# Kernel optimization log

Hardware: AMD Instinct MI355X
Metric: run time of the kernel (lower is better)

The kernel has to match this reference:

```python
import jax, jax.numpy as jnp
import numpy as np

THRESH = 0.3

def _quantize_ternary(s):
    # straight-through ternary: forward value is q, gradient is identity
    q = jnp.where(s > THRESH, 1.0, jnp.where(s < -THRESH, -1.0, 0.0))
    return s + jax.lax.stop_gradient(q - s)

def setup_inputs() -> dict:
    key = jax.random.key(0)
    k1, k2, k3 = jax.random.split(key, 3)
    B, D, T, C = 32768, 1024, 16, 1000
    x = jax.random.normal(k1, (B, D), dtype=jnp.float32)
    sigs_raw = jax.random.normal(k2, (T, D), dtype=jnp.float32) * 0.5
    # per-tile Linear(d_model, n_classes): weight [C, D], bias [C]
    W = jax.random.normal(k3, (T, C, D), dtype=jnp.float32) / np.sqrt(D)
    b = jnp.zeros((T, C), dtype=jnp.float32)
    return {"x": x, "sigs_raw": sigs_raw, "W": W, "b": b}

def reference(x, sigs_raw, W, b):
    sigs = _quantize_ternary(sigs_raw)          # [T, D] ternary values
    scores = x @ sigs.T                          # [B, T]
    tile_indices = jnp.argmax(scores, axis=-1)   # [B] top-1 routing
    n_tiles = W.shape[0]
    logits = jnp.zeros((x.shape[0], W.shape[1]), dtype=x.dtype)  # [B, C]
    # static loop over tiles: masked per-expert linear, combined by select
    for t in range(n_tiles):
        m = (tile_indices == t)[:, None]         # [B, 1]
        yt = x @ W[t].T + b[t]                   # [B, C]
        logits = jnp.where(m, yt, logits)
    return logits, tile_indices
```

## Files before the change

### kernel.cpp

```cpp
#include <hip/hip_runtime.h>

#define NBROWS 32768
#define ND 1024
#define NT 16
#define NC 1000
#define NHB 128
#define MAX_RB128 272

typedef short short8 __attribute__((ext_vector_type(8)));
typedef float f32x4 __attribute__((ext_vector_type(4)));
typedef unsigned short ushort_t;

typedef __attribute__((address_space(1))) const unsigned int* gas_t;
typedef __attribute__((address_space(3))) unsigned int* las_t;

__device__ __forceinline__ void async_copy16(const void* g, void* l) {
  __builtin_amdgcn_global_load_lds((gas_t)g, (las_t)l, 16, 0, 0);
}

__device__ __forceinline__ unsigned f2bf(float f) {
  unsigned u = __float_as_uint(f);
  u += 0x7FFFu + ((u >> 16) & 1u);
  return u >> 16;
}
__device__ __forceinline__ unsigned pk2(float a, float b) {
  return f2bf(a) | (f2bf(b) << 16);
}
__device__ __forceinline__ int swz(int row) { return (row & 3) ^ ((row >> 2) & 3); }

__global__ __launch_bounds__(512) void fused_pre(
    const float* __restrict__ x, const float* __restrict__ sigs_raw,
    int* __restrict__ tidx, float* __restrict__ out_idx,
    const float* __restrict__ W, ushort_t* __restrict__ wbf) {
  __shared__ signed char s_lds[NT * ND];
  int tid = threadIdx.x;
  int bid = blockIdx.x;
  if (bid >= 4096) {
    if (!wbf) return;
    size_t e = (((size_t)(bid - 4096)) * 512 + tid) * 8;
    int t = (int)(e >> 20);
    int rem = (int)(e & 1048575);
    int col = rem >> 10, k = rem & 1023;
    uint4 o;
    if (col < NC) {
      const float* src = W + ((size_t)t * NC + col) * ND + k;
      float4 a = *(const float4*)src;
      float4 b = *(const float4*)(src + 4);
      o = make_uint4(pk2(a.x, a.y), pk2(a.z, a.w), pk2(b.x, b.y), pk2(b.z, b.w));
    } else {
      o = make_uint4(0, 0, 0, 0);
    }
    *(uint4*)(wbf + e) = o;
    return;
  }
  for (int i = tid; i < NT * ND; i += 512) {
    float s = sigs_raw[i];
    s_lds[i] = (s > 0.3f) ? 1 : ((s < -0.3f) ? -1 : 0);
  }
  __syncthreads();
  int lane = tid & 63;
  int row = bid * 8 + (tid >> 6);
  const float* xr = x + (size_t)row * ND + lane * 16;
  float4 v0 = *(const float4*)(xr);
  float4 v1 = *(const float4*)(xr + 4);
  float4 v2 = *(const float4*)(xr + 8);
  float4 v3 = *(const float4*)(xr + 12);
  float xv[16] = {v0.x, v0.y, v0.z, v0.w, v1.x, v1.y, v1.z, v1.w,
                  v2.x, v2.y, v2.z, v2.w, v3.x, v3.y, v3.z, v3.w};
  float best = 0.0f;
  int bt = 0;
#pragma unroll
  for (int t = 0; t < NT; t++) {
    int4 sc = *(const int4*)(s_lds + t * ND + lane * 16);
    int wa[4] = {sc.x, sc.y, sc.z, sc.w};
    float p = 0.0f;
#pragma unroll
    for (int wi = 0; wi < 4; wi++)
#pragma unroll
      for (int bi = 0; bi < 4; bi++)
        p = fmaf((float)(signed char)(wa[wi] >> (8 * bi)), xv[wi * 4 + bi], p);
#pragma unroll
    for (int o = 32; o > 0; o >>= 1) p += __shfl_xor(p, o);
    if (t == 0 || p > best) { best = p; bt = t; }
  }
  if (lane == 0) {
    tidx[row] = bt;
    out_idx[row] = (float)bt;
  }
}

__global__ __launch_bounds__(256) void trix_hist(const int* __restrict__ tidx,
                                                 int* __restrict__ blkhist) {
  __shared__ int h[NT];
  int tid = threadIdx.x;
  if (tid < NT) h[tid] = 0;
  __syncthreads();
  int t = tidx[blockIdx.x * 256 + tid];
  atomicAdd(&h[t], 1);
  __syncthreads();
  if (tid < NT) blkhist[blockIdx.x * NT + tid] = h[tid];
}

__global__ __launch_bounds__(256) void trix_prefix(const int* __restrict__ blkhist,
                                                   int* __restrict__ blkbase,
                                                   int* __restrict__ meta) {
  __shared__ int part[NT][16];
  int tid = threadIdx.x;
  int t = tid >> 4, g = tid & 15;
  int s = 0;
  for (int b = g; b < NHB; b += 16) s += blkhist[b * NT + t];
  part[t][g] = s;
  __syncthreads();
  if (tid == 0) {
    int off = 0, cb2 = 0;
    for (int tt = 0; tt < NT; tt++) {
      int c = 0;
#pragma unroll
      for (int gg = 0; gg < 16; gg++) c += part[tt][gg];
      meta[tt] = c;
      meta[16 + tt] = off;
      meta[50 + tt] = cb2;
      off += c;
      cb2 += (c + 127) >> 7;
    }
    meta[32] = off;
    meta[66] = cb2;
  }
  __syncthreads();
  if (tid < NT) {
    int run = meta[16 + tid];
    for (int b = 0; b < NHB; b++) {
      blkbase[b * NT + tid] = run;
      run += blkhist[b * NT + tid];
    }
  }
}

__global__ __launch_bounds__(256) void trix_scatter(const int* __restrict__ tidx,
                                                    const int* __restrict__ blkbase,
                                                    int* __restrict__ rowlist) {
  __shared__ int h[NT];
  int tid = threadIdx.x;
  if (tid < NT) h[tid] = 0;
  __syncthreads();
  int row = blockIdx.x * 256 + tid;
  int t = tidx[row];
  int r = atomicAdd(&h[t], 1);
  rowlist[blkbase[blockIdx.x * NT + t] + r] = row;
}

__global__ __launch_bounds__(512) void trix_gather(const float* __restrict__ x,
                                                   const int* __restrict__ rowlist,
                                                   ushort_t* __restrict__ xsrt) {
  int tid = threadIdx.x;
  int lane = tid & 63, wv = tid >> 6;
  int p = blockIdx.x * 8 + wv;
  int row = rowlist[p];
  const float* src = x + (size_t)row * ND + lane * 16;
  float4 v0 = *(const float4*)(src);
  float4 v1 = *(const float4*)(src + 4);
  float4 v2 = *(const float4*)(src + 8);
  float4 v3 = *(const float4*)(src + 12);
  ushort_t* dst = xsrt + (size_t)p * ND + lane * 16;
  *(uint4*)(dst) = make_uint4(pk2(v0.x, v0.y), pk2(v0.z, v0.w), pk2(v1.x, v1.y), pk2(v1.z, v1.w));
  *(uint4*)(dst + 8) = make_uint4(pk2(v2.x, v2.y), pk2(v2.z, v2.w), pk2(v3.x, v3.y), pk2(v3.z, v3.w));
}

__global__ __launch_bounds__(256, 3) void trix_gemm4(
    const ushort_t* __restrict__ xsrt, const ushort_t* __restrict__ wbf,
    const float* __restrict__ bias, const int* __restrict__ meta,
    const int* __restrict__ rowlist, float* __restrict__ out) {
  __shared__ __align__(16) ushort_t A_lds[128 * 64];
  __shared__ __align__(16) ushort_t B_lds[128 * 64];
  __shared__ int rl[128];
  int bid = blockIdx.x;
  int w = (bid & 7) * 272 + (bid >> 3);
  int nb = w & 7, rb = w >> 3;
  if (rb >= meta[66]) return;
  int t = 0;
  while (t < NT - 1 && rb >= meta[51 + t]) t++;
  int row0 = meta[16 + t] + (rb - meta[50 + t]) * 128;
  int cnt = meta[17 + t] - row0;
  if (cnt > 128) cnt = 128;
  int tid = threadIdx.x;
  if (tid < 128) rl[tid] = rowlist[(tid < cnt) ? (row0 + tid) : row0];

  int lane = tid & 63, wv = tid >> 6;
  int srow = lane >> 3;
  int schunk = ((lane & 7) ^ srow) * 8;
  const ushort_t* aSrc = xsrt + (size_t)(row0 + wv * 32 + srow) * ND + schunk;
  const ushort_t* bSrc =
      wbf + ((size_t)t << 20) + (size_t)(nb * 128 + wv * 32 + srow) * ND + schunk;
  ushort_t* aDst = A_lds + wv * 32 * 64 + lane * 8;
  ushort_t* bDst = B_lds + wv * 32 * 64 + lane * 8;

  int wr = wv >> 1, wc = wv & 1;
  int rsel = lane & 15, ksl = lane >> 4, rx = rsel & 7;
  int sl0 = (ksl ^ rx) * 8;
  int sl1 = ((4 + ksl) ^ rx) * 8;
  int aoff = (wr * 64 + rsel) * 64;
  int boff = (wc * 64 + rsel) * 64;

  f32x4 acc[4][4] = {};

#pragma unroll 1
  for (int k0 = 0; k0 < ND; k0 += 64) {
#pragma unroll
    for (int j = 0; j < 4; j++) {
      async_copy16(aSrc + k0 + j * 8 * ND, aDst + j * 512);
      async_copy16(bSrc + k0 + j * 8 * ND, bDst + j * 512);
    }
    __syncthreads();
    short8 af[4][2], bf2[2][2];
#pragma unroll
    for (int m = 0; m < 4; m++) {
      af[m][0] = *(const short8*)(A_lds + aoff + m * 1024 + sl0);
      af[m][1] = *(const short8*)(A_lds + aoff + m * 1024 + sl1);
    }
#pragma unroll
    for (int nh = 0; nh < 2; nh++) {
#pragma unroll
      for (int j = 0; j < 2; j++) {
        int n = nh * 2 + j;
        bf2[j][0] = *(const short8*)(B_lds + boff + n * 1024 + sl0);
        bf2[j][1] = *(const short8*)(B_lds + boff + n * 1024 + sl1);
      }
#pragma unroll
      for (int m = 0; m < 4; m++)
#pragma unroll
        for (int j = 0; j < 2; j++) {
          acc[m][nh * 2 + j] = __builtin_amdgcn_mfma_f32_16x16x32_bf16(
              af[m][0], bf2[j][0], acc[m][nh * 2 + j], 0, 0, 0);
          acc[m][nh * 2 + j] = __builtin_amdgcn_mfma_f32_16x16x32_bf16(
              af[m][1], bf2[j][1], acc[m][nh * 2 + j], 0, 0, 0);
        }
    }
    __syncthreads();
  }

  float bv[4];
  int bcol[4];
#pragma unroll
  for (int n = 0; n < 4; ++n) {
    bcol[n] = nb * 128 + wc * 64 + n * 16 + rsel;
    bv[n] = (bcol[n] < NC) ? bias[t * NC + bcol[n]] : 0.0f;
  }
#pragma unroll
  for (int m = 0; m < 4; ++m) {
#pragma unroll
    for (int r = 0; r < 4; ++r) {
      int lr = wr * 64 + m * 16 + ksl * 4 + r;
      if (lr < cnt) {
        size_t ob = (size_t)rl[lr] * NC;
#pragma unroll
        for (int n = 0; n < 4; ++n)
          if (bcol[n] < NC) out[ob + bcol[n]] = acc[m][n][r] + bv[n];
      }
    }
  }
}

__global__ __launch_bounds__(256) void trix_gemm_fb(
    const float* __restrict__ x, const float* __restrict__ W,
    const float* __restrict__ bias, const int* __restrict__ meta,
    const int* __restrict__ rowlist, float* __restrict__ out) {
  __shared__ __align__(16) unsigned char aT[128 * 64];
  __shared__ __align__(16) unsigned char bT[128 * 64];
  __shared__ int rl[128];
  int nb = blockIdx.x, rb = blockIdx.y;
  if (rb >= meta[66]) return;
  int t = 0;
  while (t < NT - 1 && rb >= meta[51 + t]) t++;
  int row0 = meta[16 + t] + (rb - meta[50 + t]) * 128;
  int cnt = meta[17 + t] - row0;
  if (cnt > 128) cnt = 128;
  int tid = threadIdx.x;
  if (tid < 128) rl[tid] = rowlist[(tid < cnt) ? (row0 + tid) : row0];
  __syncthreads();
  int half = tid & 1, rloc = tid >> 1;
  const float* xp = x + (size_t)rl[rloc] * ND + half * 16;
  int wn = nb * 128 + rloc;
  if (wn > NC - 1) wn = NC - 1;
  const float* wp = W + ((size_t)t * NC + wn) * ND + half * 16;
  int sw = swz(rloc);
  unsigned char* aw0 = aT + rloc * 64 + (((half * 2 + 0) ^ sw) << 4);
  unsigned char* aw1 = aT + rloc * 64 + (((half * 2 + 1) ^ sw) << 4);
  unsigned char* bw0 = bT + rloc * 64 + (((half * 2 + 0) ^ sw) << 4);
  unsigned char* bw1 = bT + rloc * 64 + (((half * 2 + 1) ^ sw) << 4);
  int lane = tid & 63, wv = tid >> 6;
  int wr = wv >> 1, wc = wv & 1;
  int rsel = lane & 15, slot = lane >> 4;
  f32x4 acc[4][4] = {};
  for (int k0 = 0; k0 < ND; k0 += 32) {
    const float* xk = xp + k0;
    const float* wk = wp + k0;
    float4 a0 = *(const float4*)(xk);
    float4 a1 = *(const float4*)(xk + 4);
    float4 a2 = *(const float4*)(xk + 8);
    float4 a3 = *(const float4*)(xk + 12);
    float4 b0 = *(const float4*)(wk);
    float4 b1 = *(const float4*)(wk + 4);
    float4 b2 = *(const float4*)(wk + 8);
    float4 b3 = *(const float4*)(wk + 12);
    *(uint4*)aw0 = make_uint4(pk2(a0.x, a0.y), pk2(a0.z, a0.w), pk2(a1.x, a1.y), pk2(a1.z, a1.w));
    *(uint4*)aw1 = make_uint4(pk2(a2.x, a2.y), pk2(a2.z, a2.w), pk2(a3.x, a3.y), pk2(a3.z, a3.w));
    *(uint4*)bw0 = make_uint4(pk2(b0.x, b0.y), pk2(b0.z, b0.w), pk2(b1.x, b1.y), pk2(b1.z, b1.w));
    *(uint4*)bw1 = make_uint4(pk2(b2.x, b2.y), pk2(b2.z, b2.w), pk2(b3.x, b3.y), pk2(b3.z, b3.w));
    __syncthreads();
    short8 af2[4], bfr[4];
#pragma unroll
    for (int i = 0; i < 4; i++) {
      int arr = wr * 64 + i * 16 + rsel;
      af2[i] = *(const short8*)(aT + arr * 64 + ((slot ^ swz(arr)) << 4));
      int brr = wc * 64 + i * 16 + rsel;
      bfr[i] = *(const short8*)(bT + brr * 64 + ((slot ^ swz(brr)) << 4));
    }
#pragma unroll
    for (int mi = 0; mi < 4; mi++)
#pragma unroll
      for (int ni = 0; ni < 4; ni++)
        acc[mi][ni] = __builtin_amdgcn_mfma_f32_16x16x32_bf16(af2[mi], bfr[ni], acc[mi][ni], 0, 0, 0);
    __syncthreads();
  }
#pragma unroll
  for (int mi = 0; mi < 4; mi++) {
#pragma unroll
    for (int r = 0; r < 4; r++) {
      int rloc2 = wr * 64 + mi * 16 + slot * 4 + r;
      if (rloc2 < cnt) {
        size_t obase = (size_t)rl[rloc2] * NC;
#pragma unroll
        for (int ni = 0; ni < 4; ni++) {
          int col = nb * 128 + wc * 64 + ni * 16 + rsel;
          if (col < NC) out[obase + col] = acc[mi][ni][r] + bias[t * NC + col];
        }
      }
    }
  }
}

extern "C" void kernel_launch(void* const* d_in, const int* in_sizes, int n_in,
                              void* d_out, int out_size, void* d_ws, size_t ws_size,
                              hipStream_t stream) {
  const float* x = (const float*)d_in[0];
  const float* sigs = (const float*)d_in[1];
  const float* W = (const float*)d_in[2];
  const float* bias = (const float*)d_in[3];
  float* out = (float*)d_out;

  const size_t XSRT_B = (size_t)(NBROWS + 256) * ND * 2;
  const size_t WBF_B = (size_t)NT * 1024 * ND * 2;
  bool fast = ws_size >= XSRT_B + WBF_B + (1 << 20);

  char* wsb = (char*)d_ws;
  ushort_t* xsrt = nullptr;
  ushort_t* wbf = nullptr;
  int* tidx;
  if (fast) {
    xsrt = (ushort_t*)wsb;
    wbf = (ushort_t*)(wsb + XSRT_B);
    tidx = (int*)(wsb + XSRT_B + WBF_B);
  } else {
    tidx = (int*)wsb;
  }
  int* rowlist = tidx + NBROWS;
  int* meta = rowlist + NBROWS;
  int* blkhist = meta + 80;
  int* blkbase = blkhist + NHB * NT;

  fused_pre<<<8192, 512, 0, stream>>>(x, sigs, tidx, out + (size_t)NBROWS * NC, W, wbf);
  trix_hist<<<NHB, 256, 0, stream>>>(tidx, blkhist);
  trix_prefix<<<1, 256, 0, stream>>>(blkhist, blkbase, meta);
  trix_scatter<<<NHB, 256, 0, stream>>>(tidx, blkbase, rowlist);
  if (fast) {
    trix_gather<<<NBROWS / 8, 512, 0, stream>>>(x, rowlist, xsrt);
    trix_gemm4<<<8 * MAX_RB128, 256, 0, stream>>>(xsrt, wbf, bias, meta, rowlist, out);
  } else {
    trix_gemm_fb<<<dim3(8, MAX_RB128), 256, 0, stream>>>(x, W, bias, meta, rowlist, out);
  }
}
```

Measured before the change: 218.8 us.

## Fuse bf16 x conversion into routing pass and double-buffer GEMM LDS tiles

```diff
diff --git a/kernel.cpp b/kernel.cpp
--- a/kernel.cpp
+++ b/kernel.cpp
@@ -31,7 +31,8 @@
 __global__ __launch_bounds__(512) void fused_pre(
     const float* __restrict__ x, const float* __restrict__ sigs_raw,
     int* __restrict__ tidx, float* __restrict__ out_idx,
-    const float* __restrict__ W, ushort_t* __restrict__ wbf) {
+    const float* __restrict__ W, ushort_t* __restrict__ wbf,
+    ushort_t* __restrict__ xbf) {
   __shared__ signed char s_lds[NT * ND];
   int tid = threadIdx.x;
   int bid = blockIdx.x;
@@ -67,6 +68,11 @@
   float4 v3 = *(const float4*)(xr + 12);
   float xv[16] = {v0.x, v0.y, v0.z, v0.w, v1.x, v1.y, v1.z, v1.w,
                   v2.x, v2.y, v2.z, v2.w, v3.x, v3.y, v3.z, v3.w};
+  if (xbf) {
+    ushort_t* xo = xbf + (size_t)row * ND + lane * 16;
+    *(uint4*)(xo) = make_uint4(pk2(v0.x, v0.y), pk2(v0.z, v0.w), pk2(v1.x, v1.y), pk2(v1.z, v1.w));
+    *(uint4*)(xo + 8) = make_uint4(pk2(v2.x, v2.y), pk2(v2.z, v2.w), pk2(v3.x, v3.y), pk2(v3.z, v3.w));
+  }
   float best = 0.0f;
   int bt = 0;
 #pragma unroll
@@ -149,29 +155,12 @@
   rowlist[blkbase[blockIdx.x * NT + t] + r] = row;
 }
 
-__global__ __launch_bounds__(512) void trix_gather(const float* __restrict__ x,
-                                                   const int* __restrict__ rowlist,
-                                                   ushort_t* __restrict__ xsrt) {
-  int tid = threadIdx.x;
-  int lane = tid & 63, wv = tid >> 6;
-  int p = blockIdx.x * 8 + wv;
-  int row = rowlist[p];
-  const float* src = x + (size_t)row * ND + lane * 16;
-  float4 v0 = *(const float4*)(src);
-  float4 v1 = *(const float4*)(src + 4);
-  float4 v2 = *(const float4*)(src + 8);
-  float4 v3 = *(const float4*)(src + 12);
-  ushort_t* dst = xsrt + (size_t)p * ND + lane * 16;
-  *(uint4*)(dst) = make_uint4(pk2(v0.x, v0.y), pk2(v0.z, v0.w), pk2(v1.x, v1.y), pk2(v1.z, v1.w));
-  *(uint4*)(dst + 8) = make_uint4(pk2(v2.x, v2.y), pk2(v2.z, v2.w), pk2(v3.x, v3.y), pk2(v3.z, v3.w));
-}
-
-__global__ __launch_bounds__(256, 3) void trix_gemm4(
-    const ushort_t* __restrict__ xsrt, const ushort_t* __restrict__ wbf,
+__global__ __launch_bounds__(256, 2) void trix_gemm5(
+    const ushort_t* __restrict__ xbf, const ushort_t* __restrict__ wbf,
     const float* __restrict__ bias, const int* __restrict__ meta,
     const int* __restrict__ rowlist, float* __restrict__ out) {
-  __shared__ __align__(16) ushort_t A_lds[128 * 64];
-  __shared__ __align__(16) ushort_t B_lds[128 * 64];
+  __shared__ __align__(16) ushort_t A_lds[2][128 * 64];
+  __shared__ __align__(16) ushort_t B_lds[2][128 * 64];
   __shared__ int rl[128];
   int bid = blockIdx.x;
   int w = (bid & 7) * 272 + (bid >> 3);
@@ -184,15 +173,19 @@
   if (cnt > 128) cnt = 128;
   int tid = threadIdx.x;
   if (tid < 128) rl[tid] = rowlist[(tid < cnt) ? (row0 + tid) : row0];
+  __syncthreads();
 
   int lane = tid & 63, wv = tid >> 6;
   int srow = lane >> 3;
   int schunk = ((lane & 7) ^ srow) * 8;
-  const ushort_t* aSrc = xsrt + (size_t)(row0 + wv * 32 + srow) * ND + schunk;
-  const ushort_t* bSrc =
-      wbf + ((size_t)t << 20) + (size_t)(nb * 128 + wv * 32 + srow) * ND + schunk;
-  ushort_t* aDst = A_lds + wv * 32 * 64 + lane * 8;
-  ushort_t* bDst = B_lds + wv * 32 * 64 + lane * 8;
+  const ushort_t* aS[4];
+  const ushort_t* bS[4];
+#pragma unroll
+  for (int j = 0; j < 4; j++) {
+    aS[j] = xbf + (size_t)rl[wv * 32 + j * 8 + srow] * ND + schunk;
+    bS[j] = wbf + ((size_t)t << 20) + (size_t)(nb * 128 + wv * 32 + j * 8 + srow) * ND + schunk;
+  }
+  int ldst = wv * 2048 + lane * 8;
 
   int wr = wv >> 1, wc = wv & 1;
   int rsel = lane & 15, ksl = lane >> 4, rx = rsel & 7;
@@ -203,38 +196,45 @@
 
   f32x4 acc[4][4] = {};
 
+#define STAGE(DB, KTL)                                       \
+  _Pragma("unroll") for (int j = 0; j < 4; j++) {            \
+    async_copy16(aS[j] + (KTL) * 64, &A_lds[DB][ldst + j * 512]); \
+    async_copy16(bS[j] + (KTL) * 64, &B_lds[DB][ldst + j * 512]); \
+  }
+
+#define COMPUTE(DB)                                                          \
+  {                                                                          \
+    short8 af[4][2], bf2[2][2];                                              \
+    _Pragma("unroll") for (int m = 0; m < 4; m++) {                          \
+      af[m][0] = *(const short8*)(&A_lds[DB][aoff + m * 1024 + sl0]);        \
+      af[m][1] = *(const short8*)(&A_lds[DB][aoff + m * 1024 + sl1]);        \
+    }                                                                        \
+    _Pragma("unroll") for (int nh = 0; nh < 2; nh++) {                       \
+      _Pragma("unroll") for (int j = 0; j < 2; j++) {                        \
+        int n = nh * 2 + j;                                                  \
+        bf2[j][0] = *(const short8*)(&B_lds[DB][boff + n * 1024 + sl0]);     \
+        bf2[j][1] = *(const short8*)(&B_lds[DB][boff + n * 1024 + sl1]);     \
+      }                                                                      \
+      _Pragma("unroll") for (int m = 0; m < 4; m++)                          \
+          _Pragma("unroll") for (int j = 0; j < 2; j++) {                    \
+        acc[m][nh * 2 + j] = __builtin_amdgcn_mfma_f32_16x16x32_bf16(        \
+            af[m][0], bf2[j][0], acc[m][nh * 2 + j], 0, 0, 0);               \
+        acc[m][nh * 2 + j] = __builtin_amdgcn_mfma_f32_16x16x32_bf16(        \
+            af[m][1], bf2[j][1], acc[m][nh * 2 + j], 0, 0, 0);               \
+      }                                                                      \
+    }                                                                        \
+  }
+
+  STAGE(0, 0);
+  __syncthreads();
+
 #pragma unroll 1
-  for (int k0 = 0; k0 < ND; k0 += 64) {
-#pragma unroll
-    for (int j = 0; j < 4; j++) {
-      async_copy16(aSrc + k0 + j * 8 * ND, aDst + j * 512);
-      async_copy16(bSrc + k0 + j * 8 * ND, bDst + j * 512);
-    }
+  for (int kt = 0; kt < 8; ++kt) {
+    STAGE(1, 2 * kt + 1);
+    COMPUTE(0);
     __syncthreads();
-    short8 af[4][2], bf2[2][2];
-#pragma unroll
-    for (int m = 0; m < 4; m++) {
-      af[m][0] = *(const short8*)(A_lds + aoff + m * 1024 + sl0);
-      af[m][1] = *(const short8*)(A_lds + aoff + m * 1024 + sl1);
-    }
-#pragma unroll
-    for (int nh = 0; nh < 2; nh++) {
-#pragma unroll
-      for (int j = 0; j < 2; j++) {
-        int n = nh * 2 + j;
-        bf2[j][0] = *(const short8*)(B_lds + boff + n * 1024 + sl0);
-        bf2[j][1] = *(const short8*)(B_lds + boff + n * 1024 + sl1);
-      }
-#pragma unroll
-      for (int m = 0; m < 4; m++)
-#pragma unroll
-        for (int j = 0; j < 2; j++) {
-          acc[m][nh * 2 + j] = __builtin_amdgcn_mfma_f32_16x16x32_bf16(
-              af[m][0], bf2[j][0], acc[m][nh * 2 + j], 0, 0, 0);
-          acc[m][nh * 2 + j] = __builtin_amdgcn_mfma_f32_16x16x32_bf16(
-              af[m][1], bf2[j][1], acc[m][nh * 2 + j], 0, 0, 0);
-        }
-    }
+    if (kt < 7) STAGE(0, 2 * kt + 2);
+    COMPUTE(1);
     __syncthreads();
   }
 
@@ -258,6 +258,8 @@
       }
     }
   }
+#undef STAGE
+#undef COMPUTE
 }
 
 __global__ __launch_bounds__(256) void trix_gemm_fb(
@@ -348,18 +350,18 @@
   const float* bias = (const float*)d_in[3];
   float* out = (float*)d_out;
 
-  const size_t XSRT_B = (size_t)(NBROWS + 256) * ND * 2;
+  const size_t XBF_B = (size_t)NBROWS * ND * 2;
   const size_t WBF_B = (size_t)NT * 1024 * ND * 2;
-  bool fast = ws_size >= XSRT_B + WBF_B + (1 << 20);
+  bool fast = ws_size >= XBF_B + WBF_B + (1 << 20);
 
   char* wsb = (char*)d_ws;
-  ushort_t* xsrt = nullptr;
+  ushort_t* xbf = nullptr;
   ushort_t* wbf = nullptr;
   int* tidx;
   if (fast) {
-    xsrt = (ushort_t*)wsb;
-    wbf = (ushort_t*)(wsb + XSRT_B);
-    tidx = (int*)(wsb + XSRT_B + WBF_B);
+    xbf = (ushort_t*)wsb;
+    wbf = (ushort_t*)(wsb + XBF_B);
+    tidx = (int*)(wsb + XBF_B + WBF_B);
   } else {
     tidx = (int*)wsb;
   }
@@ -368,13 +370,12 @@
   int* blkhist = meta + 80;
   int* blkbase = blkhist + NHB * NT;
 
-  fused_pre<<<8192, 512, 0, stream>>>(x, sigs, tidx, out + (size_t)NBROWS * NC, W, wbf);
+  fused_pre<<<8192, 512, 0, stream>>>(x, sigs, tidx, out + (size_t)NBROWS * NC, W, wbf, xbf);
   trix_hist<<<NHB, 256, 0, stream>>>(tidx, blkhist);
   trix_prefix<<<1, 256, 0, stream>>>(blkhist, blkbase, meta);
   trix_scatter<<<NHB, 256, 0, stream>>>(tidx, blkbase, rowlist);
   if (fast) {
-    trix_gather<<<NBROWS / 8, 512, 0, stream>>>(x, rowlist, xsrt);
-    trix_gemm4<<<8 * MAX_RB128, 256, 0, stream>>>(xsrt, wbf, bias, meta, rowlist, out);
+    trix_gemm5<<<8 * MAX_RB128, 256, 0, stream>>>(xbf, wbf, bias, meta, rowlist, out);
   } else {
     trix_gemm_fb<<<dim3(8, MAX_RB128), 256, 0, stream>>>(x, W, bias, meta, rowlist, out);
   }
```

After: 204.2 us. 1.07x faster.

## Fuse bf16 conversion of x into routing kernel and gather rows in GEMM

Applied to the files above, without the earlier changes.

```diff
diff --git a/kernel.cpp b/kernel.cpp
--- a/kernel.cpp
+++ b/kernel.cpp
@@ -31,7 +31,8 @@
 __global__ __launch_bounds__(512) void fused_pre(
     const float* __restrict__ x, const float* __restrict__ sigs_raw,
     int* __restrict__ tidx, float* __restrict__ out_idx,
-    const float* __restrict__ W, ushort_t* __restrict__ wbf) {
+    const float* __restrict__ W, ushort_t* __restrict__ wbf,
+    ushort_t* __restrict__ xbf) {
   __shared__ signed char s_lds[NT * ND];
   int tid = threadIdx.x;
   int bid = blockIdx.x;
@@ -67,6 +68,11 @@
   float4 v3 = *(const float4*)(xr + 12);
   float xv[16] = {v0.x, v0.y, v0.z, v0.w, v1.x, v1.y, v1.z, v1.w,
                   v2.x, v2.y, v2.z, v2.w, v3.x, v3.y, v3.z, v3.w};
+  if (xbf) {
+    ushort_t* xo = xbf + (size_t)row * ND + lane * 16;
+    *(uint4*)(xo) = make_uint4(pk2(v0.x, v0.y), pk2(v0.z, v0.w), pk2(v1.x, v1.y), pk2(v1.z, v1.w));
+    *(uint4*)(xo + 8) = make_uint4(pk2(v2.x, v2.y), pk2(v2.z, v2.w), pk2(v3.x, v3.y), pk2(v3.z, v3.w));
+  }
   float best = 0.0f;
   int bt = 0;
 #pragma unroll
@@ -149,25 +155,8 @@
   rowlist[blkbase[blockIdx.x * NT + t] + r] = row;
 }
 
-__global__ __launch_bounds__(512) void trix_gather(const float* __restrict__ x,
-                                                   const int* __restrict__ rowlist,
-                                                   ushort_t* __restrict__ xsrt) {
-  int tid = threadIdx.x;
-  int lane = tid & 63, wv = tid >> 6;
-  int p = blockIdx.x * 8 + wv;
-  int row = rowlist[p];
-  const float* src = x + (size_t)row * ND + lane * 16;
-  float4 v0 = *(const float4*)(src);
-  float4 v1 = *(const float4*)(src + 4);
-  float4 v2 = *(const float4*)(src + 8);
-  float4 v3 = *(const float4*)(src + 12);
-  ushort_t* dst = xsrt + (size_t)p * ND + lane * 16;
-  *(uint4*)(dst) = make_uint4(pk2(v0.x, v0.y), pk2(v0.z, v0.w), pk2(v1.x, v1.y), pk2(v1.z, v1.w));
-  *(uint4*)(dst + 8) = make_uint4(pk2(v2.x, v2.y), pk2(v2.z, v2.w), pk2(v3.x, v3.y), pk2(v3.z, v3.w));
-}
-
-__global__ __launch_bounds__(256, 3) void trix_gemm4(
-    const ushort_t* __restrict__ xsrt, const ushort_t* __restrict__ wbf,
+__global__ __launch_bounds__(256, 3) void trix_gemm6(
+    const ushort_t* __restrict__ xbf, const ushort_t* __restrict__ wbf,
     const float* __restrict__ bias, const int* __restrict__ meta,
     const int* __restrict__ rowlist, float* __restrict__ out) {
   __shared__ __align__(16) ushort_t A_lds[128 * 64];
@@ -184,15 +173,19 @@
   if (cnt > 128) cnt = 128;
   int tid = threadIdx.x;
   if (tid < 128) rl[tid] = rowlist[(tid < cnt) ? (row0 + tid) : row0];
+  __syncthreads();
 
   int lane = tid & 63, wv = tid >> 6;
   int srow = lane >> 3;
   int schunk = ((lane & 7) ^ srow) * 8;
-  const ushort_t* aSrc = xsrt + (size_t)(row0 + wv * 32 + srow) * ND + schunk;
-  const ushort_t* bSrc =
-      wbf + ((size_t)t << 20) + (size_t)(nb * 128 + wv * 32 + srow) * ND + schunk;
-  ushort_t* aDst = A_lds + wv * 32 * 64 + lane * 8;
-  ushort_t* bDst = B_lds + wv * 32 * 64 + lane * 8;
+  const ushort_t* aS[4];
+  const ushort_t* bS[4];
+#pragma unroll
+  for (int j = 0; j < 4; j++) {
+    aS[j] = xbf + (size_t)rl[wv * 32 + j * 8 + srow] * ND + schunk;
+    bS[j] = wbf + ((size_t)t << 20) + (size_t)(nb * 128 + wv * 32 + j * 8 + srow) * ND + schunk;
+  }
+  int ldst = wv * 2048 + lane * 8;
 
   int wr = wv >> 1, wc = wv & 1;
   int rsel = lane & 15, ksl = lane >> 4, rx = rsel & 7;
@@ -207,23 +200,23 @@
   for (int k0 = 0; k0 < ND; k0 += 64) {
 #pragma unroll
     for (int j = 0; j < 4; j++) {
-      async_copy16(aSrc + k0 + j * 8 * ND, aDst + j * 512);
-      async_copy16(bSrc + k0 + j * 8 * ND, bDst + j * 512);
+      async_copy16(aS[j] + k0, &A_lds[ldst + j * 512]);
+      async_copy16(bS[j] + k0, &B_lds[ldst + j * 512]);
     }
     __syncthreads();
     short8 af[4][2], bf2[2][2];
 #pragma unroll
     for (int m = 0; m < 4; m++) {
-      af[m][0] = *(const short8*)(A_lds + aoff + m * 1024 + sl0);
-      af[m][1] = *(const short8*)(A_lds + aoff + m * 1024 + sl1);
+      af[m][0] = *(const short8*)(&A_lds[aoff + m * 1024 + sl0]);
+      af[m][1] = *(const short8*)(&A_lds[aoff + m * 1024 + sl1]);
     }
 #pragma unroll
     for (int nh = 0; nh < 2; nh++) {
 #pragma unroll
       for (int j = 0; j < 2; j++) {
         int n = nh * 2 + j;
-        bf2[j][0] = *(const short8*)(B_lds + boff + n * 1024 + sl0);
-        bf2[j][1] = *(const short8*)(B_lds + boff + n * 1024 + sl1);
+        bf2[j][0] = *(const short8*)(&B_lds[boff + n * 1024 + sl0]);
+        bf2[j][1] = *(const short8*)(&B_lds[boff + n * 1024 + sl1]);
       }
 #pragma unroll
       for (int m = 0; m < 4; m++)
@@ -348,18 +341,18 @@
   const float* bias = (const float*)d_in[3];
   float* out = (float*)d_out;
 
-  const size_t XSRT_B = (size_t)(NBROWS + 256) * ND * 2;
+  const size_t XBF_B = (size_t)NBROWS * ND * 2;
   const size_t WBF_B = (size_t)NT * 1024 * ND * 2;
-  bool fast = ws_size >= XSRT_B + WBF_B + (1 << 20);
+  bool fast = ws_size >= XBF_B + WBF_B + (1 << 20);
 
   char* wsb = (char*)d_ws;
-  ushort_t* xsrt = nullptr;
+  ushort_t* xbf = nullptr;
   ushort_t* wbf = nullptr;
   int* tidx;
   if (fast) {
-    xsrt = (ushort_t*)wsb;
-    wbf = (ushort_t*)(wsb + XSRT_B);
-    tidx = (int*)(wsb + XSRT_B + WBF_B);
+    xbf = (ushort_t*)wsb;
+    wbf = (ushort_t*)(wsb + XBF_B);
+    tidx = (int*)(wsb + XBF_B + WBF_B);
   } else {
     tidx = (int*)wsb;
   }
@@ -368,13 +361,12 @@
   int* blkhist = meta + 80;
   int* blkbase = blkhist + NHB * NT;
 
-  fused_pre<<<8192, 512, 0, stream>>>(x, sigs, tidx, out + (size_t)NBROWS * NC, W, wbf);
+  fused_pre<<<8192, 512, 0, stream>>>(x, sigs, tidx, out + (size_t)NBROWS * NC, W, wbf, xbf);
   trix_hist<<<NHB, 256, 0, stream>>>(tidx, blkhist);
   trix_prefix<<<1, 256, 0, stream>>>(blkhist, blkbase, meta);
   trix_scatter<<<NHB, 256, 0, stream>>>(tidx, blkbase, rowlist);
   if (fast) {
-    trix_gather<<<NBROWS / 8, 512, 0, stream>>>(x, rowlist, xsrt);
-    trix_gemm4<<<8 * MAX_RB128, 256, 0, stream>>>(xsrt, wbf, bias, meta, rowlist, out);
+    trix_gemm6<<<8 * MAX_RB128, 256, 0, stream>>>(xbf, wbf, bias, meta, rowlist, out);
   } else {
     trix_gemm_fb<<<dim3(8, MAX_RB128), 256, 0, stream>>>(x, W, bias, meta, rowlist, out);
   }
```

After: 179.7 us. 1.22x faster.
